# Performance work log

Measured on AMD Instinct MI355X. Metric: run time of the kernel, lower is better.

The kernel has to match this reference:

```python
import jax, jax.numpy as jnp
import numpy as np

N_NODES = 50000
N_EDGES = 800000
D_IN, D_HID, D_OUT = 128, 256, 256


def _mean_agg(h_src, src, dst, n_nodes):
    # gather source features along edges, segment-sum into dst, divide by in-degree
    gathered = h_src[src]                                        # [E, d]
    sums = jax.ops.segment_sum(gathered, dst, num_segments=n_nodes)  # [N, d]
    deg = jax.ops.segment_sum(jnp.ones((src.shape[0],), h_src.dtype), dst,
                              num_segments=n_nodes)              # [N]
    return sums / jnp.clip(deg, 1.0)[:, None]


def setup_inputs() -> dict:
    key = jax.random.key(0)
    ks = jax.random.split(key, 10)
    s = 0.05
    return {
        "x": jax.random.normal(ks[0], (N_NODES, D_IN), jnp.float32),
        "src": jax.random.randint(ks[1], (N_EDGES,), 0, N_NODES, jnp.int32),
        "dst": jax.random.randint(ks[2], (N_EDGES,), 0, N_NODES, jnp.int32),
        "W_self1": jax.random.normal(ks[3], (D_IN, D_HID), jnp.float32) * s,
        "W_neigh1": jax.random.normal(ks[4], (D_IN, D_HID), jnp.float32) * s,
        "b1": jnp.zeros((D_HID,), jnp.float32),
        "W_self2": jax.random.normal(ks[5], (D_HID, D_OUT), jnp.float32) * s,
        "W_neigh2": jax.random.normal(ks[6], (D_HID, D_OUT), jnp.float32) * s,
        "b2": jnp.zeros((D_OUT,), jnp.float32),
        "W_res": jax.random.normal(ks[7], (D_IN, D_OUT), jnp.float32) * s,
        "W_mlp": jax.random.normal(ks[8], (D_OUT, 2), jnp.float32) * s,
        "b_mlp": jnp.zeros((2,), jnp.float32),
    }


def reference(x, src, dst, W_self1, W_neigh1, b1, W_self2, W_neigh2, b2,
              W_res, W_mlp, b_mlp):
    n = x.shape[0]
    # SAGEConv 1 (mean aggregator) + ReLU (dropout p=0.0 is identity)
    h = x @ W_self1 + _mean_agg(x, src, dst, n) @ W_neigh1 + b1
    h = jax.nn.relu(h)
    # SAGEConv 2
    h = h @ W_self2 + _mean_agg(h, src, dst, n) @ W_neigh2 + b2
    # residual connection
    h = h + x @ W_res
    # MLP head
    return h @ W_mlp + b_mlp
```

## Files before the change

kernel.cpp:

```cpp
#include <hip/hip_runtime.h>

#define N_NODES 50000
#define N_EDGES 800000
#define D_IN 128
#define D_HID 256
#define D_OUT 256

#define SCAN_BLOCKS ((N_NODES + 255) / 256)
#define NXB ((N_NODES + 127) / 128)
#define M_PAD (NXB * 128)

using short8 = __attribute__((ext_vector_type(8))) short;
using f32x4  = __attribute__((ext_vector_type(4))) float;

__device__ inline unsigned short f2bf(float f) {
    unsigned u = __float_as_uint(f);
    u += 0x7fff + ((u >> 16) & 1);
    return (unsigned short)(u >> 16);
}
__device__ inline float bf2f(unsigned v16) {
    return __uint_as_float(v16 << 16);
}

__device__ inline void gload_lds16(const void* g, void* l) {
    __builtin_amdgcn_global_load_lds(
        (const __attribute__((address_space(1))) unsigned int*)g,
        (__attribute__((address_space(3))) unsigned int*)l, 16, 0, 0);
}


__global__ void hist_kernel(const int* __restrict__ dst, int* __restrict__ cnt) {
    int e = blockIdx.x * blockDim.x + threadIdx.x;
    if (e < N_EDGES) atomicAdd(&cnt[dst[e]], 1);
}

__global__ __launch_bounds__(256) void scan1_kernel(const int* __restrict__ cnt,
                                                    int* __restrict__ blocksum) {
    int i = blockIdx.x * 256 + threadIdx.x;
    int v = (i < N_NODES) ? cnt[i] : 0;
    int lane = threadIdx.x & 63, wid = threadIdx.x >> 6;
    for (int off = 32; off; off >>= 1) v += __shfl_down(v, off);
    __shared__ int ws[4];
    if (lane == 0) ws[wid] = v;
    __syncthreads();
    if (threadIdx.x == 0) blocksum[blockIdx.x] = ws[0] + ws[1] + ws[2] + ws[3];
}

__global__ __launch_bounds__(256) void scan2_kernel(const int* __restrict__ blocksum,
                                                    int* __restrict__ blockoff) {
    int tid = threadIdx.x;
    int lane = tid & 63, wid = tid >> 6;
    int v = (tid < SCAN_BLOCKS) ? blocksum[tid] : 0;
    int inc = v;
    for (int off = 1; off < 64; off <<= 1) {
        int u = __shfl_up(inc, off);
        if (lane >= off) inc += u;
    }
    __shared__ int ws[4];
    if (lane == 63) ws[wid] = inc;
    __syncthreads();
    int base = 0;
    for (int w = 0; w < wid; ++w) base += ws[w];
    if (tid < SCAN_BLOCKS) blockoff[tid] = base + inc - v;
}

__global__ __launch_bounds__(256) void scan3_kernel(const int* __restrict__ cnt,
                                                    const int* __restrict__ blockoff,
                                                    int* __restrict__ row_ptr,
                                                    int* __restrict__ cursor,
                                                    float* __restrict__ inv_deg) {
    int i = blockIdx.x * 256 + threadIdx.x;
    int c = (i < N_NODES) ? cnt[i] : 0;
    int lane = threadIdx.x & 63, wid = threadIdx.x >> 6;
    int inc = c;
    for (int off = 1; off < 64; off <<= 1) {
        int u = __shfl_up(inc, off);
        if (lane >= off) inc += u;
    }
    __shared__ int ws[4];
    if (lane == 63) ws[wid] = inc;
    __syncthreads();
    int base = blockoff[blockIdx.x];
    for (int w = 0; w < wid; ++w) base += ws[w];
    if (i < N_NODES) {
        int pos = base + inc - c;
        row_ptr[i] = pos;
        cursor[i] = pos;
        inv_deg[i] = 1.0f / (float)max(c, 1);
    }
    if (i == 0) row_ptr[N_NODES] = N_EDGES;
}

__global__ void fill_kernel(const int* __restrict__ src, const int* __restrict__ dst,
                            int* __restrict__ cursor, int* __restrict__ srcs) {
    int e = blockIdx.x * blockDim.x + threadIdx.x;
    if (e < N_EDGES) {
        int pos = atomicAdd(&cursor[dst[e]], 1);
        srcs[pos] = src[e];
    }
}


__global__ void convx_kernel(const float* __restrict__ x,
                             unsigned short* __restrict__ A1,
                             unsigned short* __restrict__ A2) {
    int idx = blockIdx.x * 256 + threadIdx.x;
    if (idx >= N_NODES * D_IN) return;
    int n = idx >> 7, k = idx & 127;
    unsigned short b = f2bf(x[idx]);
    A1[(long)n * 256 + k] = b;
    A2[(long)n * 640 + 512 + k] = b;
}

__global__ void wconv1_kernel(const float* __restrict__ Ws, const float* __restrict__ Wn,
                              unsigned short* __restrict__ Wt) {
    int j = blockIdx.x;
    for (int k = threadIdx.x; k < 256; k += 256) {
        float v = (k < 128) ? Ws[k * 256 + j] : Wn[(k - 128) * 256 + j];
        Wt[j * 256 + k] = f2bf(v);
    }
}

__global__ void wconv2_kernel(const float* __restrict__ Ws, const float* __restrict__ Wn,
                              const float* __restrict__ Wr,
                              unsigned short* __restrict__ Wt) {
    int j = blockIdx.x;
    for (int k = threadIdx.x; k < 640; k += 256) {
        float v = (k < 256) ? Ws[k * 256 + j]
                : (k < 512) ? Wn[(k - 256) * 256 + j]
                            : Wr[(k - 512) * 256 + j];
        Wt[j * 640 + k] = f2bf(v);
    }
}


__global__ void agg1_kernel(const int* __restrict__ row_ptr,
                            const int* __restrict__ srcs,
                            const float* __restrict__ inv_deg,
                            unsigned short* __restrict__ A1) {
    int n = blockIdx.x;
    int tid = threadIdx.x;
    int beg = row_ptr[n], end = row_ptr[n + 1];
    float acc = 0.f;
    int e = beg;
    for (; e + 3 < end; e += 4) {
        int s0 = srcs[e], s1 = srcs[e + 1], s2 = srcs[e + 2], s3 = srcs[e + 3];
        unsigned v0 = A1[(long)s0 * 256 + tid];
        unsigned v1 = A1[(long)s1 * 256 + tid];
        unsigned v2 = A1[(long)s2 * 256 + tid];
        unsigned v3 = A1[(long)s3 * 256 + tid];
        acc += (bf2f(v0) + bf2f(v1)) + (bf2f(v2) + bf2f(v3));
    }
    for (; e < end; ++e) acc += bf2f((unsigned)A1[(long)srcs[e] * 256 + tid]);
    A1[(long)n * 256 + 128 + tid] = f2bf(acc * inv_deg[n]);
}

__global__ void agg2_kernel(unsigned short* __restrict__ A2,
                            const int* __restrict__ row_ptr,
                            const int* __restrict__ srcs,
                            const float* __restrict__ inv_deg) {
    int n = blockIdx.x;
    int tid = threadIdx.x;
    int beg = row_ptr[n], end = row_ptr[n + 1];
    float a0 = 0.f, a1 = 0.f;
    int e = beg;
    for (; e + 3 < end; e += 4) {
        int s0 = srcs[e], s1 = srcs[e + 1], s2 = srcs[e + 2], s3 = srcs[e + 3];
        unsigned v0 = ((const unsigned*)(A2 + (long)s0 * 640))[tid];
        unsigned v1 = ((const unsigned*)(A2 + (long)s1 * 640))[tid];
        unsigned v2 = ((const unsigned*)(A2 + (long)s2 * 640))[tid];
        unsigned v3 = ((const unsigned*)(A2 + (long)s3 * 640))[tid];
        a0 += (bf2f(v0 & 0xffffu) + bf2f(v1 & 0xffffu)) +
              (bf2f(v2 & 0xffffu) + bf2f(v3 & 0xffffu));
        a1 += (bf2f(v0 >> 16) + bf2f(v1 >> 16)) + (bf2f(v2 >> 16) + bf2f(v3 >> 16));
    }
    for (; e < end; ++e) {
        unsigned v = ((const unsigned*)(A2 + (long)srcs[e] * 640))[tid];
        a0 += bf2f(v & 0xffffu);
        a1 += bf2f(v >> 16);
    }
    float inv = inv_deg[n];
    unsigned o = (unsigned)f2bf(a0 * inv) | ((unsigned)f2bf(a1 * inv) << 16);
    ((unsigned*)(A2 + (long)n * 640 + 256))[tid] = o;
}


template <int K, bool RELU>
__global__ __launch_bounds__(256) void gemm97_kernel(
    const unsigned short* __restrict__ A, const unsigned short* __restrict__ Bt,
    const float* __restrict__ bias, unsigned short* __restrict__ out, int outStride) {
    __shared__ unsigned short As[128 * 32];
    __shared__ unsigned short Bs[128 * 32];

    int tid = threadIdx.x;
    int lane = tid & 63, w = tid >> 6;

    constexpr int NWG = NXB * 2;
    constexpr int Q = NWG / 8, R = NWG % 8;
    int b = blockIdx.x;
    int xcd = b & 7, slot = b >> 3;
    int l = (xcd < R) ? xcd * (Q + 1) + slot : R * (Q + 1) + (xcd - R) * Q + slot;
    int bx = l >> 1, by = l & 1;

    int row0 = bx * 128, col0 = by * 128;
    int wr = (w >> 1) * 64, wc = (w & 1) * 64;
    int l15 = lane & 15, kg = (lane >> 4) * 8;

    f32x4 acc[4][4] = {};

    int e0 = w * 64 + lane;
    int e1 = 256 + e0;
    int r0 = e0 >> 2, c80 = e0 & 3;
    int r1 = e1 >> 2, c81 = e1 & 3;

    const unsigned short* gA0 = A + (long)(row0 + r0) * K + c80 * 8;
    const unsigned short* gA1 = A + (long)(row0 + r1) * K + c81 * 8;
    const unsigned short* gB0 = Bt + (long)(col0 + r0) * K + c80 * 8;
    const unsigned short* gB1 = Bt + (long)(col0 + r1) * K + c81 * 8;
    unsigned short* lA0 = &As[e0 * 8];
    unsigned short* lA1 = &As[e1 * 8];
    unsigned short* lB0 = &Bs[e0 * 8];
    unsigned short* lB1 = &Bs[e1 * 8];

    for (int kc = 0; kc < K; kc += 32) {
        gload_lds16(gA0 + kc, lA0);
        gload_lds16(gA1 + kc, lA1);
        gload_lds16(gB0 + kc, lB0);
        gload_lds16(gB1 + kc, lB1);
        __syncthreads();

        short8 a[4], bq[4];
#pragma unroll
        for (int i = 0; i < 4; ++i) {
            a[i]  = *(const short8*)(&As[(wr + 16 * i + l15) * 32 + kg]);
            bq[i] = *(const short8*)(&Bs[(wc + 16 * i + l15) * 32 + kg]);
        }
#pragma unroll
        for (int i = 0; i < 4; ++i)
#pragma unroll
            for (int j = 0; j < 4; ++j)
                acc[i][j] = __builtin_amdgcn_mfma_f32_16x16x32_bf16(a[i], bq[j], acc[i][j], 0, 0, 0);
        __syncthreads();
    }

#pragma unroll
    for (int j = 0; j < 4; ++j) {
        int c = col0 + wc + 16 * j + l15;
        float bv = bias[c];
#pragma unroll
        for (int i = 0; i < 4; ++i) {
            int rbase = row0 + wr + 16 * i + (lane >> 4) * 4;
#pragma unroll
            for (int r = 0; r < 4; ++r) {
                int row = rbase + r;
                if (row < N_NODES) {
                    float v = acc[i][j][r] + bv;
                    if (RELU) v = fmaxf(v, 0.f);
                    out[(long)row * outStride + c] = f2bf(v);
                }
            }
        }
    }
}


__global__ __launch_bounds__(256) void head_kernel(const unsigned short* __restrict__ h2,
                                                   const float* __restrict__ Wmlp,
                                                   const float* __restrict__ bmlp,
                                                   float* __restrict__ out) {
    int n = blockIdx.x * 4 + (threadIdx.x >> 6);
    int lane = threadIdx.x & 63;
    const unsigned* p = (const unsigned*)(h2 + (long)n * 256 + lane * 4);
    unsigned v0 = p[0], v1 = p[1];
    float f0 = bf2f(v0 & 0xffffu), f1 = bf2f(v0 >> 16);
    float f2 = bf2f(v1 & 0xffffu), f3 = bf2f(v1 >> 16);
    int k = lane * 4;
    float p0 = f0 * Wmlp[k * 2]       + f1 * Wmlp[(k + 1) * 2]
             + f2 * Wmlp[(k + 2) * 2] + f3 * Wmlp[(k + 3) * 2];
    float p1 = f0 * Wmlp[k * 2 + 1]       + f1 * Wmlp[(k + 1) * 2 + 1]
             + f2 * Wmlp[(k + 2) * 2 + 1] + f3 * Wmlp[(k + 3) * 2 + 1];
    for (int off = 32; off; off >>= 1) {
        p0 += __shfl_down(p0, off);
        p1 += __shfl_down(p1, off);
    }
    if (lane == 0) {
        out[(long)n * 2]     = p0 + bmlp[0];
        out[(long)n * 2 + 1] = p1 + bmlp[1];
    }
}


extern "C" void kernel_launch(void* const* d_in, const int* in_sizes, int n_in,
                              void* d_out, int out_size, void* d_ws, size_t ws_size,
                              hipStream_t stream) {
    const float* x    = (const float*)d_in[0];
    const int*   src  = (const int*)d_in[1];
    const int*   dst  = (const int*)d_in[2];
    const float* Ws1  = (const float*)d_in[3];
    const float* Wn1  = (const float*)d_in[4];
    const float* b1   = (const float*)d_in[5];
    const float* Ws2  = (const float*)d_in[6];
    const float* Wn2  = (const float*)d_in[7];
    const float* b2   = (const float*)d_in[8];
    const float* Wres = (const float*)d_in[9];
    const float* Wmlp = (const float*)d_in[10];
    const float* bmlp = (const float*)d_in[11];
    float* out = (float*)d_out;

    char* ws = (char*)d_ws;
    size_t off = 0;
    auto alloc = [&](size_t bytes) {
        void* p = ws + off;
        off += (bytes + 255) & ~(size_t)255;
        return p;
    };
    int*            cnt      = (int*)alloc((size_t)N_NODES * 4);
    int*            row_ptr  = (int*)alloc((size_t)(N_NODES + 1) * 4);
    int*            cursor   = (int*)alloc((size_t)N_NODES * 4);
    float*          inv_deg  = (float*)alloc((size_t)N_NODES * 4);
    int*            srcs     = (int*)alloc((size_t)N_EDGES * 4);
    int*            blocksum = (int*)alloc((size_t)SCAN_BLOCKS * 4);
    int*            blockoff = (int*)alloc((size_t)SCAN_BLOCKS * 4);
    unsigned short* A1       = (unsigned short*)alloc((size_t)M_PAD * 256 * 2);
    unsigned short* A2       = (unsigned short*)alloc((size_t)M_PAD * 640 * 2);
    unsigned short* Wt1      = (unsigned short*)alloc((size_t)256 * 256 * 2);
    unsigned short* Wt2      = (unsigned short*)alloc((size_t)256 * 640 * 2);

    hipMemsetAsync(cnt, 0, (size_t)N_NODES * 4, stream);
    hist_kernel<<<(N_EDGES + 255) / 256, 256, 0, stream>>>(dst, cnt);
    scan1_kernel<<<SCAN_BLOCKS, 256, 0, stream>>>(cnt, blocksum);
    scan2_kernel<<<1, 256, 0, stream>>>(blocksum, blockoff);
    scan3_kernel<<<SCAN_BLOCKS, 256, 0, stream>>>(cnt, blockoff, row_ptr, cursor, inv_deg);
    fill_kernel<<<(N_EDGES + 255) / 256, 256, 0, stream>>>(src, dst, cursor, srcs);
    convx_kernel<<<(N_NODES * D_IN + 255) / 256, 256, 0, stream>>>(x, A1, A2);
    wconv1_kernel<<<256, 256, 0, stream>>>(Ws1, Wn1, Wt1);
    wconv2_kernel<<<256, 256, 0, stream>>>(Ws2, Wn2, Wres, Wt2);
    agg1_kernel<<<N_NODES, 128, 0, stream>>>(row_ptr, srcs, inv_deg, A1);

    gemm97_kernel<256, true><<<NXB * 2, 256, 0, stream>>>(A1, Wt1, b1, A2, 640);
    agg2_kernel<<<N_NODES, 128, 0, stream>>>(A2, row_ptr, srcs, inv_deg);
    gemm97_kernel<640, false><<<NXB * 2, 256, 0, stream>>>(A2, Wt2, b2, A1, 256);
    head_kernel<<<N_NODES / 4, 256, 0, stream>>>(A1, Wmlp, bmlp, out);
}
```

Baseline: 378.7 us.

## Fuse MLP head into second GEMM epilogue and widen K tile with swizzled LDS

The GEMM now stages 64-wide K chunks instead of 32, halving the number of barrier pairs per tile, and XOR-swizzles the LDS layout to avoid bank conflicts on the MFMA fragment reads. The second GEMM no longer writes the bf16 hidden state. It computes the 256x2 MLP head dot products in its epilogue, reduces them with lane shuffles, and atomically adds partial results into a pre-zeroed output. This removes the head kernel launch and the write and re-read of the hidden state, at the cost of a memset, float atomics (nondeterministic summation order), and doubled LDS per block.

New measurement: 359.2 us. 5.1% less time.

```diff
diff --git a/kernel.cpp b/kernel.cpp
--- a/kernel.cpp
+++ b/kernel.cpp
@@ -185,12 +185,14 @@
 }
 
 
-template <int K, bool RELU>
+template <int K, bool RELU, bool HEAD>
 __global__ __launch_bounds__(256) void gemm97_kernel(
     const unsigned short* __restrict__ A, const unsigned short* __restrict__ Bt,
-    const float* __restrict__ bias, unsigned short* __restrict__ out, int outStride) {
-    __shared__ unsigned short As[128 * 32];
-    __shared__ unsigned short Bs[128 * 32];
+    const float* __restrict__ bias, unsigned short* __restrict__ out, int outStride,
+    const float* __restrict__ Wmlp, const float* __restrict__ bmlp,
+    float* __restrict__ outF) {
+    __shared__ unsigned short As[128 * 64];
+    __shared__ unsigned short Bs[128 * 64];
 
     int tid = threadIdx.x;
     int lane = tid & 63, w = tid >> 6;
@@ -204,88 +206,107 @@
 
     int row0 = bx * 128, col0 = by * 128;
     int wr = (w >> 1) * 64, wc = (w & 1) * 64;
-    int l15 = lane & 15, kg = (lane >> 4) * 8;
+    int l15 = lane & 15, g = lane >> 4;
 
     f32x4 acc[4][4] = {};
 
-    int e0 = w * 64 + lane;
-    int e1 = 256 + e0;
-    int r0 = e0 >> 2, c80 = e0 & 3;
-    int r1 = e1 >> 2, c81 = e1 & 3;
-
-    const unsigned short* gA0 = A + (long)(row0 + r0) * K + c80 * 8;
-    const unsigned short* gA1 = A + (long)(row0 + r1) * K + c81 * 8;
-    const unsigned short* gB0 = Bt + (long)(col0 + r0) * K + c80 * 8;
-    const unsigned short* gB1 = Bt + (long)(col0 + r1) * K + c81 * 8;
-    unsigned short* lA0 = &As[e0 * 8];
-    unsigned short* lA1 = &As[e1 * 8];
-    unsigned short* lB0 = &Bs[e0 * 8];
-    unsigned short* lB1 = &Bs[e1 * 8];
-
-    for (int kc = 0; kc < K; kc += 32) {
-        gload_lds16(gA0 + kc, lA0);
-        gload_lds16(gA1 + kc, lA1);
-        gload_lds16(gB0 + kc, lB0);
-        gload_lds16(gB1 + kc, lB1);
+    const unsigned short* gA[4];
+    const unsigned short* gB[4];
+    unsigned short* lA[4];
+    unsigned short* lB[4];
+#pragma unroll
+    for (int q = 0; q < 4; ++q) {
+        int e = q * 256 + tid;
+        int r = e >> 3, s = e & 7;
+        int ks = s ^ (r & 7);
+        gA[q] = A + (long)(row0 + r) * K + ks * 8;
+        gB[q] = Bt + (long)(col0 + r) * K + ks * 8;
+        lA[q] = &As[e * 8];
+        lB[q] = &Bs[e * 8];
+    }
+    int p0s = (0 * 4 + g) ^ (l15 & 7);
+    int p1s = (1 * 4 + g) ^ (l15 & 7);
+
+    for (int kc = 0; kc < K; kc += 64) {
+#pragma unroll
+        for (int q = 0; q < 4; ++q) gload_lds16(gA[q] + kc, lA[q]);
+#pragma unroll
+        for (int q = 0; q < 4; ++q) gload_lds16(gB[q] + kc, lB[q]);
         __syncthreads();
 
-        short8 a[4], bq[4];
-#pragma unroll
-        for (int i = 0; i < 4; ++i) {
-            a[i]  = *(const short8*)(&As[(wr + 16 * i + l15) * 32 + kg]);
-            bq[i] = *(const short8*)(&Bs[(wc + 16 * i + l15) * 32 + kg]);
+#pragma unroll
+        for (int t = 0; t < 2; ++t) {
+            int ps = t ? p1s : p0s;
+            short8 a[4], bq[4];
+#pragma unroll
+            for (int i = 0; i < 4; ++i) {
+                int ra = wr + 16 * i + l15;
+                int rbq = wc + 16 * i + l15;
+                a[i]  = *(const short8*)(&As[ra * 64 + ps * 8]);
+                bq[i] = *(const short8*)(&Bs[rbq * 64 + ps * 8]);
+            }
+#pragma unroll
+            for (int i = 0; i < 4; ++i)
+#pragma unroll
+                for (int j = 0; j < 4; ++j)
+                    acc[i][j] = __builtin_amdgcn_mfma_f32_16x16x32_bf16(a[i], bq[j], acc[i][j], 0, 0, 0);
         }
-#pragma unroll
-        for (int i = 0; i < 4; ++i)
-#pragma unroll
-            for (int j = 0; j < 4; ++j)
-                acc[i][j] = __builtin_amdgcn_mfma_f32_16x16x32_bf16(a[i], bq[j], acc[i][j], 0, 0, 0);
         __syncthreads();
     }
 
-#pragma unroll
-    for (int j = 0; j < 4; ++j) {
-        int c = col0 + wc + 16 * j + l15;
-        float bv = bias[c];
-#pragma unroll
-        for (int i = 0; i < 4; ++i) {
-            int rbase = row0 + wr + 16 * i + (lane >> 4) * 4;
-#pragma unroll
-            for (int r = 0; r < 4; ++r) {
-                int row = rbase + r;
-                if (row < N_NODES) {
-                    float v = acc[i][j][r] + bv;
-                    if (RELU) v = fmaxf(v, 0.f);
-                    out[(long)row * outStride + c] = f2bf(v);
+    if (!HEAD) {
+#pragma unroll
+        for (int j = 0; j < 4; ++j) {
+            int c = col0 + wc + 16 * j + l15;
+            float bv = bias[c];
+#pragma unroll
+            for (int i = 0; i < 4; ++i) {
+                int rbase = row0 + wr + 16 * i + g * 4;
+#pragma unroll
+                for (int r = 0; r < 4; ++r) {
+                    int row = rbase + r;
+                    if (row < N_NODES) {
+                        float v = acc[i][j][r] + bv;
+                        if (RELU) v = fmaxf(v, 0.f);
+                        out[(long)row * outStride + c] = f2bf(v);
+                    }
                 }
             }
         }
-    }
-}
-
-
-__global__ __launch_bounds__(256) void head_kernel(const unsigned short* __restrict__ h2,
-                                                   const float* __restrict__ Wmlp,
-                                                   const float* __restrict__ bmlp,
-                                                   float* __restrict__ out) {
-    int n = blockIdx.x * 4 + (threadIdx.x >> 6);
-    int lane = threadIdx.x & 63;
-    const unsigned* p = (const unsigned*)(h2 + (long)n * 256 + lane * 4);
-    unsigned v0 = p[0], v1 = p[1];
-    float f0 = bf2f(v0 & 0xffffu), f1 = bf2f(v0 >> 16);
-    float f2 = bf2f(v1 & 0xffffu), f3 = bf2f(v1 >> 16);
-    int k = lane * 4;
-    float p0 = f0 * Wmlp[k * 2]       + f1 * Wmlp[(k + 1) * 2]
-             + f2 * Wmlp[(k + 2) * 2] + f3 * Wmlp[(k + 3) * 2];
-    float p1 = f0 * Wmlp[k * 2 + 1]       + f1 * Wmlp[(k + 1) * 2 + 1]
-             + f2 * Wmlp[(k + 2) * 2 + 1] + f3 * Wmlp[(k + 3) * 2 + 1];
-    for (int off = 32; off; off >>= 1) {
-        p0 += __shfl_down(p0, off);
-        p1 += __shfl_down(p1, off);
-    }
-    if (lane == 0) {
-        out[(long)n * 2]     = p0 + bmlp[0];
-        out[(long)n * 2 + 1] = p1 + bmlp[1];
+    } else {
+        float bv[4], wm0[4], wm1[4];
+#pragma unroll
+        for (int j = 0; j < 4; ++j) {
+            int c = col0 + wc + 16 * j + l15;
+            bv[j] = bias[c];
+            wm0[j] = Wmlp[c * 2];
+            wm1[j] = Wmlp[c * 2 + 1];
+        }
+        bool lead = (by == 0) && (wc == 0);
+        float bm0 = bmlp[0], bm1 = bmlp[1];
+#pragma unroll
+        for (int i = 0; i < 4; ++i) {
+            int rbase = row0 + wr + 16 * i + g * 4;
+#pragma unroll
+            for (int r = 0; r < 4; ++r) {
+                float s0 = 0.f, s1 = 0.f;
+#pragma unroll
+                for (int j = 0; j < 4; ++j) {
+                    float h = acc[i][j][r] + bv[j];
+                    s0 += h * wm0[j];
+                    s1 += h * wm1[j];
+                }
+                for (int off = 1; off < 16; off <<= 1) {
+                    s0 += __shfl_xor(s0, off);
+                    s1 += __shfl_xor(s1, off);
+                }
+                int row = rbase + r;
+                if (l15 == 0 && row < N_NODES) {
+                    atomicAdd(&outF[(long)row * 2],     s0 + (lead ? bm0 : 0.f));
+                    atomicAdd(&outF[(long)row * 2 + 1], s1 + (lead ? bm1 : 0.f));
+                }
+            }
+        }
     }
 }
 
@@ -327,6 +348,7 @@
     unsigned short* Wt2      = (unsigned short*)alloc((size_t)256 * 640 * 2);
 
     hipMemsetAsync(cnt, 0, (size_t)N_NODES * 4, stream);
+    hipMemsetAsync(out, 0, (size_t)N_NODES * 2 * 4, stream);
     hist_kernel<<<(N_EDGES + 255) / 256, 256, 0, stream>>>(dst, cnt);
     scan1_kernel<<<SCAN_BLOCKS, 256, 0, stream>>>(cnt, blocksum);
     scan2_kernel<<<1, 256, 0, stream>>>(blocksum, blockoff);
@@ -337,8 +359,9 @@
     wconv2_kernel<<<256, 256, 0, stream>>>(Ws2, Wn2, Wres, Wt2);
     agg1_kernel<<<N_NODES, 128, 0, stream>>>(row_ptr, srcs, inv_deg, A1);
 
-    gemm97_kernel<256, true><<<NXB * 2, 256, 0, stream>>>(A1, Wt1, b1, A2, 640);
+    gemm97_kernel<256, true, false><<<NXB * 2, 256, 0, stream>>>(
+        A1, Wt1, b1, A2, 640, nullptr, nullptr, nullptr);
     agg2_kernel<<<N_NODES, 128, 0, stream>>>(A2, row_ptr, srcs, inv_deg);
-    gemm97_kernel<640, false><<<NXB * 2, 256, 0, stream>>>(A2, Wt2, b2, A1, 256);
-    head_kernel<<<N_NODES / 4, 256, 0, stream>>>(A1, Wmlp, bmlp, out);
-}
+    gemm97_kernel<640, false, true><<<NXB * 2, 256, 0, stream>>>(
+        A2, Wt2, b2, nullptr, 0, Wmlp, bmlp, out);
+}
```
